# Kernel optimization log

Measured on AMD Instinct MI355X. Metric: run time of the kernel, lower is better.

Reference implementation:

```python
import jax, jax.numpy as jnp
import numpy as np

D_MODEL = 1024
N_HEADS = 16
MIXTURE_FACTOR = 4
LATENT = D_MODEL // MIXTURE_FACTOR  # 256
D_K = D_MODEL // N_HEADS            # 64
B, L = 2, 2048


def setup_inputs() -> dict:
    key = jax.random.key(0)
    ks = jax.random.split(key, 13)
    s_in = 1.0 / np.sqrt(D_MODEL)
    s_lat = 1.0 / np.sqrt(LATENT)
    return {
        "queries": jax.random.normal(ks[0], (B, L, 1, D_MODEL), jnp.float32),
        "keys": jax.random.normal(ks[1], (B, L, 1, D_MODEL), jnp.float32),
        "values": jax.random.normal(ks[2], (B, L, 1, D_MODEL), jnp.float32),
        "Wq": jax.random.normal(ks[3], (D_MODEL, D_MODEL), jnp.float32) * s_in,
        "bq": jnp.zeros((D_MODEL,), jnp.float32),
        "Wd": jax.random.normal(ks[4], (D_MODEL, LATENT), jnp.float32) * s_in,
        "bd": jnp.zeros((LATENT,), jnp.float32),
        "Wk": jax.random.normal(ks[5], (LATENT, D_MODEL), jnp.float32) * s_lat,
        "bk": jnp.zeros((D_MODEL,), jnp.float32),
        "Wv": jax.random.normal(ks[6], (LATENT, D_MODEL), jnp.float32) * s_lat,
        "bv": jnp.zeros((D_MODEL,), jnp.float32),
        "Wo": jax.random.normal(ks[7], (D_MODEL, D_MODEL), jnp.float32) * s_in,
        "bo": jnp.zeros((D_MODEL,), jnp.float32),
    }


def reference(queries, keys, values, Wq, bq, Wd, bd, Wk, bk, Wv, bv, Wo, bo):
    b, l, h_in, e = queries.shape  # h_in == 1, e == d_model
    s = keys.shape[1]
    scale = D_K ** -0.5

    q_flat = queries.reshape(b, l, e)
    Q = (q_flat @ Wq + bq).reshape(b, l, N_HEADS, D_K)

    kv_input = keys.reshape(b, s, e)
    latent = kv_input @ Wd + bd                      # [b, s, latent]
    K = (latent @ Wk + bk).reshape(b, s, N_HEADS, D_K)
    V = (latent @ Wv + bv).reshape(b, s, N_HEADS, D_K)

    scores = jnp.einsum('blhe,bshe->bhls', Q, K) * scale  # [b, h, l, s]
    causal = jnp.triu(jnp.ones((l, s), dtype=bool), k=1)
    scores = jnp.where(causal, -jnp.inf, scores)
    A = jax.nn.softmax(scores, axis=-1)

    out = jnp.einsum('bhls,bshd->blhd', A, V).reshape(b, l, N_HEADS * D_K)
    return out @ Wo + bo
```

## Files before the change

### kernel.cpp

```cpp
#include <hip/hip_runtime.h>
#include <stdint.h>


#define DM 1024
#define NH 16
#define DK 64
#define LL 2048

typedef float  f32x4  __attribute__((ext_vector_type(4)));
typedef __bf16 bf16x8 __attribute__((ext_vector_type(8)));
typedef short  s16x8  __attribute__((ext_vector_type(8)));

__device__ __forceinline__ unsigned short f2bf(float f) {
    union { float f; unsigned int u; } v; v.f = f;
    return (unsigned short)((v.u + 0x7fffu + ((v.u >> 16) & 1u)) >> 16);
}
__device__ __forceinline__ unsigned int pack2(float a, float b) {
    return (unsigned int)f2bf(a) | ((unsigned int)f2bf(b) << 16);
}
__device__ __forceinline__ bf16x8 ld8(const unsigned short* p) {
    s16x8 s = *(const s16x8*)p;
    return __builtin_bit_cast(bf16x8, s);
}
__device__ __forceinline__ void gl16(const void* g, void* l) {
    __builtin_amdgcn_global_load_lds((__attribute__((address_space(1))) void*)(g),
                                     (__attribute__((address_space(3))) void*)(l),
                                     16, 0, 0);
}

__global__ __launch_bounds__(256)
void prep_k(const float* __restrict__ Wq, const float* __restrict__ Wd,
            const float* __restrict__ Wk, const float* __restrict__ Wv,
            const float* __restrict__ Wo, const float* __restrict__ queries,
            const float* __restrict__ keys,
            unsigned short* __restrict__ WqT, unsigned short* __restrict__ WdT,
            unsigned short* __restrict__ WkvT, unsigned short* __restrict__ WoT,
            unsigned short* __restrict__ Qb, unsigned short* __restrict__ Kb) {
    int bid = blockIdx.x;
    const int t = threadIdx.x;

    const float* W; unsigned short* WT; int TK, TN;
    if (bid < 1024)      { W = Wq; WT = WqT;  TK = 1024; TN = 1024; }
    else if (bid < 1280) { bid -= 1024; W = Wd; WT = WdT; TK = 1024; TN = 256; }
    else if (bid < 1536) { bid -= 1280; W = Wk; WT = WkvT; TK = 256; TN = 1024; }
    else if (bid < 1792) { bid -= 1536; W = Wv; WT = WkvT + (size_t)1024 * 256; TK = 256; TN = 1024; }
    else if (bid < 2816) { bid -= 1792; W = Wo; WT = WoT;  TK = 1024; TN = 1024; }
    else {
        bid -= 2816;
        const float* src; unsigned short* dst;
        if (bid < 1024) { src = queries; dst = Qb; }
        else            { bid -= 1024; src = keys; dst = Kb; }
        const size_t base = (size_t)bid * 4096;
#pragma unroll
        for (int i = 0; i < 4; ++i) {
            float4 f = *(const float4*)(src + base + (size_t)(i * 256 + t) * 4);
            uint2 u = { pack2(f.x, f.y), pack2(f.z, f.w) };
            *(uint2*)(dst + base + (size_t)(i * 256 + t) * 4) = u;
        }
        return;
    }
    __shared__ float tile[32][33];
    const int tx = t & 31, ty = t >> 5;
    const int bx = bid % (TK / 32), by = bid / (TK / 32);
    const int k0 = bx * 32, n0 = by * 32;
#pragma unroll
    for (int i = 0; i < 4; ++i)
        tile[ty + 8 * i][tx] = W[(size_t)(k0 + ty + 8 * i) * TN + n0 + tx];
    __syncthreads();
#pragma unroll
    for (int i = 0; i < 4; ++i)
        WT[(size_t)(n0 + ty + 8 * i) * TK + k0 + tx] = f2bf(tile[tx][ty + 8 * i]);
}

template<int MODE>
__global__ __launch_bounds__(256)
void gemm_k(const unsigned short* __restrict__ Ap, const unsigned short* __restrict__ Bt,
            const float* __restrict__ bias, void* __restrict__ Cp,
            const unsigned short* __restrict__ Ap2, const unsigned short* __restrict__ Bt2,
            const float* __restrict__ bias2, void* __restrict__ Cp2,
            int K) {
    __shared__ unsigned short Sh[12288];
    unsigned short* As = Sh;
    unsigned short* Bs = Sh + 8192;

    int bid = blockIdx.x;
    const unsigned short* A;
    const unsigned short* B;
    const float* bs;
    bool second = false;
    int m0, n0;
    if (MODE == 0 && bid >= 512) {
        bid -= 512; A = Ap2; B = Bt2; bs = bias2; second = true;
        const int xcd = bid & 7, s = bid >> 3;
        n0 = (s & 3) * 64; m0 = (xcd * 4 + (s >> 2)) * 128;
    } else {
        A = Ap; B = Bt; bs = bias;
        const int xcd = bid & 7, s = bid >> 3;
        if (MODE == 2) { n0 = (s & 31) * 64; m0 = (xcd * 4 + (s >> 5)) * 128; }
        else           { n0 = (s & 15) * 64; m0 = (xcd * 4 + (s >> 4)) * 128; }
    }

    const int t = threadIdx.x, lane = t & 63, wv = t >> 6;
    const int quad = lane >> 4, l15 = lane & 15;

    const int lr8 = lane >> 3;
    const int g8 = (lane & 7) ^ (lr8 & 7);
    const unsigned short* gA = A + (size_t)(m0 + wv * 32 + lr8) * K + g8 * 8;
    const unsigned short* gB = B + (size_t)(n0 + wv * 16 + lr8) * K + g8 * 8;
    unsigned short* lA = As + wv * 2048;
    unsigned short* lB = Bs + wv * 1024;

    int aoff[4][2], boff[2][2];
#pragma unroll
    for (int i = 0; i < 4; ++i) {
        const int ra = (wv >> 1) * 64 + i * 16 + l15;
#pragma unroll
        for (int ks = 0; ks < 2; ++ks)
            aoff[i][ks] = ra * 64 + (((ks * 4 + quad) ^ (ra & 7)) << 3);
    }
#pragma unroll
    for (int j = 0; j < 2; ++j) {
        const int rb = (wv & 1) * 32 + j * 16 + l15;
#pragma unroll
        for (int ks = 0; ks < 2; ++ks)
            boff[j][ks] = rb * 64 + (((ks * 4 + quad) ^ (rb & 7)) << 3);
    }

    f32x4 acc[4][2] = {};
    for (int kk = 0; kk < K; kk += 64) {
        __syncthreads();
#pragma unroll
        for (int s = 0; s < 4; ++s) gl16(gA + kk + (size_t)s * 8 * K, lA + s * 512);
#pragma unroll
        for (int s = 0; s < 2; ++s) gl16(gB + kk + (size_t)s * 8 * K, lB + s * 512);
        __syncthreads();
#pragma unroll
        for (int ks = 0; ks < 2; ++ks) {
            bf16x8 a[4], b[2];
#pragma unroll
            for (int i = 0; i < 4; ++i) a[i] = ld8(As + aoff[i][ks]);
#pragma unroll
            for (int j = 0; j < 2; ++j) b[j] = ld8(Bs + boff[j][ks]);
#pragma unroll
            for (int i = 0; i < 4; ++i)
#pragma unroll
                for (int j = 0; j < 2; ++j)
                    acc[i][j] = __builtin_amdgcn_mfma_f32_16x16x32_bf16(a[i], b[j], acc[i][j], 0, 0, 0);
        }
    }

    const bool isV = (MODE == 2) && (n0 >= 1024);
    if (!isV) {
#pragma unroll
        for (int j = 0; j < 2; ++j) {
            const int col = n0 + (wv & 1) * 32 + j * 16 + l15;
            const float bvv = bs[col];
            const int cstride = second ? 256 : 1024;
#pragma unroll
            for (int i = 0; i < 2; ++i) {}
#pragma unroll
            for (int i = 0; i < 4; ++i) {
                const int rowb = m0 + (wv >> 1) * 64 + i * 16 + quad * 4;
#pragma unroll
                for (int r = 0; r < 4; ++r) {
                    const float v = acc[i][j][r] + bvv;
                    const int row = rowb + r;
                    if (MODE == 1)
                        ((float*)Cp)[(size_t)row * 1024 + col] = v;
                    else if (second)
                        ((unsigned short*)Cp2)[(size_t)row * 256 + col] = f2bf(v);
                    else
                        ((unsigned short*)Cp)[(size_t)row * 1024 + col] = f2bf(v);
                }
            }
        }
    } else {
        __syncthreads();
        unsigned short* Ld = Sh;
#pragma unroll
        for (int j = 0; j < 2; ++j) {
            const int dloc = (wv & 1) * 32 + j * 16 + l15;
            const float bvv = bias2[(n0 - 1024) + dloc];
#pragma unroll
            for (int i = 0; i < 4; ++i) {
                const int tokb = (wv >> 1) * 64 + i * 16 + quad * 4;
#pragma unroll
                for (int r = 0; r < 4; ++r)
                    Ld[dloc * 136 + tokb + r] = f2bf(acc[i][j][r] + bvv);
            }
        }
        __syncthreads();
        const int dloc = t >> 2;
        const int tk0 = (t & 3) * 32;
        const int bb = m0 >> 11;
        unsigned short* dst = (unsigned short*)Cp2 +
            ((size_t)bb * 1024 + (n0 - 1024) + dloc) * LL + (m0 & (LL - 1)) + tk0;
        const unsigned short* srcp = Ld + dloc * 136 + tk0;
#pragma unroll
        for (int c = 0; c < 4; ++c)
            *(uint4*)(dst + c * 8) = *(const uint4*)(srcp + c * 8);
    }
}

__global__ __launch_bounds__(512)
void attn6_k(const unsigned short* __restrict__ Qp,
             const unsigned short* __restrict__ Kp,
             const unsigned short* __restrict__ VpT,
             unsigned short* __restrict__ Op) {
    __shared__ unsigned short Ks[2][4096];
    __shared__ unsigned short Vs[2][4096];
    __shared__ unsigned short Ps[8][16][72];

    const int t = threadIdx.x, lane = t & 63, wv = t >> 6;
    const int grp = wv >> 2, w4 = wv & 3;
    const int quad = lane >> 4, l15 = lane & 15;

    const int bid = blockIdx.x;
    const int xcd = bid & 7, s = bid >> 3;
    const int pair = s & 15;
    const int combo = xcd * 4 + (s >> 4);
    const int h = combo & 15, b = combo >> 4;

    const int srow = w4 * 16 + (lane >> 3);
    const int g8 = (lane & 7) ^ ((lane >> 3) & 7);
    unsigned short* lK = &Ks[grp][w4 * 1024];
    unsigned short* lV = &Vs[grp][w4 * 1024];
    const int sw = l15 & 7;
    float* cb = (float*)&Ks[0][0];

    for (int tsel = 0; tsel < 2; ++tsel) {
        const int tile = tsel ? (31 - pair) : pair;
        const int q0 = tile * 64;

        const unsigned short* qp = Qp + (size_t)(b * LL + q0 + w4 * 16 + l15) * DM + h * DK;
        const bf16x8 aq0 = ld8(qp + quad * 8);
        const bf16x8 aq1 = ld8(qp + 32 + quad * 8);

        f32x4 acc[4] = {};
        float lrow[4] = {0.f, 0.f, 0.f, 0.f};
        const int rowq = q0 + w4 * 16 + quad * 4;

        const int nit = tile / 2 + 1;
        for (int it = 0; it < nit; ++it) {
            const int c = 2 * it + grp;
            const bool active = (c <= tile);
            const int kt = c * 64;
            __syncthreads();
            if (active) {
                const unsigned short* kg = Kp + (size_t)(b * LL + kt + srow) * DM + h * DK + g8 * 8;
                const unsigned short* vg = VpT + ((size_t)(b * NH + h) * DK + srow) * LL + kt + g8 * 8;
                gl16(kg, lK);             gl16(kg + (size_t)8 * DM, lK + 512);
                gl16(vg, lV);             gl16(vg + (size_t)8 * LL, lV + 512);
            }
            __syncthreads();
            if (!active) continue;

            f32x4 s4[4];
#pragma unroll
            for (int sub = 0; sub < 4; ++sub) {
                const int base = (sub * 16 + l15) * 64;
                f32x4 ss = {};
                bf16x8 b0 = ld8(&Ks[grp][base + ((quad ^ sw) << 3)]);
                ss = __builtin_amdgcn_mfma_f32_16x16x32_bf16(aq0, b0, ss, 0, 0, 0);
                bf16x8 b1 = ld8(&Ks[grp][base + (((4 + quad) ^ sw) << 3)]);
                ss = __builtin_amdgcn_mfma_f32_16x16x32_bf16(aq1, b1, ss, 0, 0, 0);
                s4[sub] = ss;
            }

            if (c == tile) {
#pragma unroll
                for (int sub = 0; sub < 4; ++sub) {
                    const int col = kt + sub * 16 + l15;
#pragma unroll
                    for (int r = 0; r < 4; ++r) {
                        float e = exp2f(fmaf(s4[sub][r], 0.18033688011112042f, -16.0f));
                        if (col > rowq + r) e = 0.f;
                        lrow[r] += e;
                        Ps[wv][quad * 4 + r][sub * 16 + l15] =
                            (unsigned short)(__builtin_bit_cast(unsigned int, e) >> 16);
                    }
                }
            } else {
#pragma unroll
                for (int sub = 0; sub < 4; ++sub) {
#pragma unroll
                    for (int r = 0; r < 4; ++r) {
                        float e = exp2f(fmaf(s4[sub][r], 0.18033688011112042f, -16.0f));
                        lrow[r] += e;
                        Ps[wv][quad * 4 + r][sub * 16 + l15] =
                            (unsigned short)(__builtin_bit_cast(unsigned int, e) >> 16);
                    }
                }
            }

#pragma unroll
            for (int ks = 0; ks < 2; ++ks) {
                bf16x8 ap = ld8(&Ps[wv][l15][ks * 32 + quad * 8]);
#pragma unroll
                for (int sub = 0; sub < 4; ++sub) {
                    bf16x8 bv = ld8(&Vs[grp][(sub * 16 + l15) * 64 + (((ks * 4 + quad) ^ sw) << 3)]);
                    acc[sub] = __builtin_amdgcn_mfma_f32_16x16x32_bf16(ap, bv, acc[sub], 0, 0, 0);
                }
            }
        }

        __syncthreads();
        const int base = (w4 * 64 + lane) * 20;
        if (grp == 1) {
#pragma unroll
            for (int sub = 0; sub < 4; ++sub)
#pragma unroll
                for (int r = 0; r < 4; ++r) cb[base + sub * 4 + r] = acc[sub][r];
#pragma unroll
            for (int r = 0; r < 4; ++r) cb[base + 16 + r] = lrow[r];
        }
        __syncthreads();
        if (grp == 0) {
#pragma unroll
            for (int sub = 0; sub < 4; ++sub)
#pragma unroll
                for (int r = 0; r < 4; ++r) acc[sub][r] += cb[base + sub * 4 + r];
#pragma unroll
            for (int r = 0; r < 4; ++r) {
                lrow[r] += cb[base + 16 + r];
#pragma unroll
                for (int off = 1; off < 16; off <<= 1)
                    lrow[r] += __shfl_xor(lrow[r], off, 64);
                lrow[r] = __builtin_amdgcn_rcpf(lrow[r]);
            }
#pragma unroll
            for (int sub = 0; sub < 4; ++sub)
#pragma unroll
                for (int r = 0; r < 4; ++r)
                    Op[(size_t)(b * LL + rowq + r) * DM + h * DK + sub * 16 + l15] =
                        f2bf(acc[sub][r] * lrow[r]);
        }
    }
}

extern "C" void kernel_launch(void* const* d_in, const int* in_sizes, int n_in,
                              void* d_out, int out_size, void* d_ws, size_t ws_size,
                              hipStream_t stream) {
    const float* queries = (const float*)d_in[0];
    const float* keys    = (const float*)d_in[1];
    const float* Wq = (const float*)d_in[3];  const float* bq = (const float*)d_in[4];
    const float* Wd = (const float*)d_in[5];  const float* bd = (const float*)d_in[6];
    const float* Wk = (const float*)d_in[7];  const float* bk = (const float*)d_in[8];
    const float* Wv = (const float*)d_in[9];  const float* bv = (const float*)d_in[10];
    const float* Wo = (const float*)d_in[11]; const float* bo = (const float*)d_in[12];

    char* ws = (char*)d_ws;
    const size_t MB = 1048576;
    unsigned short* Qp   = (unsigned short*)(ws);
    unsigned short* Kb   = (unsigned short*)(ws + 8 * MB);
    unsigned short* Kp   = (unsigned short*)(ws + 8 * MB);
    unsigned short* Qb   = (unsigned short*)(ws + 16 * MB);
    unsigned short* VpT  = (unsigned short*)(ws + 16 * MB);
    unsigned short* WqT  = (unsigned short*)(ws + 24 * MB);
    unsigned short* Lat  = (unsigned short*)(ws + 26 * MB);
    unsigned short* WdT  = (unsigned short*)(ws + 28 * MB);
    unsigned short* WkvT = (unsigned short*)(ws + 28 * MB + 524288);
    unsigned short* Attn = (unsigned short*)(ws + 24 * MB);
    unsigned short* WoT  = (unsigned short*)(ws + 32 * MB);

    prep_k<<<4864, 256, 0, stream>>>(Wq, Wd, Wk, Wv, Wo, queries, keys,
                                     WqT, WdT, WkvT, WoT, Qb, Kb);
    gemm_k<0><<<640, 256, 0, stream>>>(Qb, WqT, bq, Qp, Kb, WdT, bd, Lat, 1024);
    gemm_k<2><<<1024, 256, 0, stream>>>(Lat, WkvT, bk, Kp, nullptr, nullptr, bv, VpT, 256);
    attn6_k<<<512, 512, 0, stream>>>(Qp, Kp, VpT, Attn);
    gemm_k<1><<<512, 256, 0, stream>>>(Attn, WoT, bo, d_out, nullptr, nullptr, nullptr, nullptr, 1024);
}
```

Before: 205.5 us.

## Double-buffer LDS tiles in GEMM kernel to overlap global loads with MFMA

Replaces the single shared-memory tile in the GEMM kernel with two ping-pong buffers. The load of the next K-slice is issued before the MFMA work on the current one, and the loop keeps one barrier per step instead of two. This is meant to hide global-to-LDS latency behind compute. In exchange, LDS use per block doubles, which may lower occupancy, and the unused cstride code is dropped.

Measured after the change: 198.8 us. 1.03x faster.

```diff
diff --git a/kernel.cpp b/kernel.cpp
--- a/kernel.cpp
+++ b/kernel.cpp
@@ -72,6 +72,33 @@
         WT[(size_t)(n0 + ty + 8 * i) * TK + k0 + tx] = f2bf(tile[tx][ty + 8 * i]);
 }
 
+__device__ __forceinline__ void stage6(const unsigned short* gA, const unsigned short* gB,
+                                       int kk, int K,
+                                       unsigned short* lA, unsigned short* lB) {
+#pragma unroll
+    for (int s = 0; s < 4; ++s) gl16(gA + kk + (size_t)s * 8 * K, lA + s * 512);
+#pragma unroll
+    for (int s = 0; s < 2; ++s) gl16(gB + kk + (size_t)s * 8 * K, lB + s * 512);
+}
+
+__device__ __forceinline__ void mfma16(const unsigned short* As, const unsigned short* Bs,
+                                       const int aoff[4][2], const int boff[2][2],
+                                       f32x4 acc[4][2]) {
+#pragma unroll
+    for (int ks = 0; ks < 2; ++ks) {
+        bf16x8 a[4], b[2];
+#pragma unroll
+        for (int i = 0; i < 4; ++i) a[i] = ld8(As + aoff[i][ks]);
+#pragma unroll
+        for (int j = 0; j < 2; ++j) b[j] = ld8(Bs + boff[j][ks]);
+#pragma unroll
+        for (int i = 0; i < 4; ++i)
+#pragma unroll
+            for (int j = 0; j < 2; ++j)
+                acc[i][j] = __builtin_amdgcn_mfma_f32_16x16x32_bf16(a[i], b[j], acc[i][j], 0, 0, 0);
+    }
+}
+
 template<int MODE>
 __global__ __launch_bounds__(256)
 void gemm_k(const unsigned short* __restrict__ Ap, const unsigned short* __restrict__ Bt,
@@ -79,9 +106,8 @@
             const unsigned short* __restrict__ Ap2, const unsigned short* __restrict__ Bt2,
             const float* __restrict__ bias2, void* __restrict__ Cp2,
             int K) {
-    __shared__ unsigned short Sh[12288];
-    unsigned short* As = Sh;
-    unsigned short* Bs = Sh + 8192;
+    __shared__ unsigned short Sh0[12288];
+    __shared__ unsigned short Sh1[12288];
 
     int bid = blockIdx.x;
     const unsigned short* A;
@@ -107,8 +133,10 @@
     const int g8 = (lane & 7) ^ (lr8 & 7);
     const unsigned short* gA = A + (size_t)(m0 + wv * 32 + lr8) * K + g8 * 8;
     const unsigned short* gB = B + (size_t)(n0 + wv * 16 + lr8) * K + g8 * 8;
-    unsigned short* lA = As + wv * 2048;
-    unsigned short* lB = Bs + wv * 1024;
+    unsigned short* lA0 = Sh0 + wv * 2048;
+    unsigned short* lB0 = Sh0 + 8192 + wv * 1024;
+    unsigned short* lA1 = Sh1 + wv * 2048;
+    unsigned short* lB1 = Sh1 + 8192 + wv * 1024;
 
     int aoff[4][2], boff[2][2];
 #pragma unroll
@@ -127,25 +155,19 @@
     }
 
     f32x4 acc[4][2] = {};
-    for (int kk = 0; kk < K; kk += 64) {
+    const int niter = K >> 6;
+
+    stage6(gA, gB, 0, K, lA0, lB0);
+    __syncthreads();
+    for (int it = 0; it < niter; it += 2) {
+        const int kk = it << 6;
+        if (it + 1 < niter) stage6(gA, gB, kk + 64, K, lA1, lB1);
+        mfma16(Sh0, Sh0 + 8192, aoff, boff, acc);
         __syncthreads();
-#pragma unroll
-        for (int s = 0; s < 4; ++s) gl16(gA + kk + (size_t)s * 8 * K, lA + s * 512);
-#pragma unroll
-        for (int s = 0; s < 2; ++s) gl16(gB + kk + (size_t)s * 8 * K, lB + s * 512);
-        __syncthreads();
-#pragma unroll
-        for (int ks = 0; ks < 2; ++ks) {
-            bf16x8 a[4], b[2];
-#pragma unroll
-            for (int i = 0; i < 4; ++i) a[i] = ld8(As + aoff[i][ks]);
-#pragma unroll
-            for (int j = 0; j < 2; ++j) b[j] = ld8(Bs + boff[j][ks]);
-#pragma unroll
-            for (int i = 0; i < 4; ++i)
-#pragma unroll
-                for (int j = 0; j < 2; ++j)
-                    acc[i][j] = __builtin_amdgcn_mfma_f32_16x16x32_bf16(a[i], b[j], acc[i][j], 0, 0, 0);
+        if (it + 1 < niter) {
+            if (it + 2 < niter) stage6(gA, gB, kk + 128, K, lA0, lB0);
+            mfma16(Sh1, Sh1 + 8192, aoff, boff, acc);
+            __syncthreads();
         }
     }
 
@@ -155,9 +177,6 @@
         for (int j = 0; j < 2; ++j) {
             const int col = n0 + (wv & 1) * 32 + j * 16 + l15;
             const float bvv = bs[col];
-            const int cstride = second ? 256 : 1024;
-#pragma unroll
-            for (int i = 0; i < 2; ++i) {}
 #pragma unroll
             for (int i = 0; i < 4; ++i) {
                 const int rowb = m0 + (wv >> 1) * 64 + i * 16 + quad * 4;
@@ -175,8 +194,7 @@
             }
         }
     } else {
-        __syncthreads();
-        unsigned short* Ld = Sh;
+        unsigned short* Ld = Sh0;
 #pragma unroll
         for (int j = 0; j < 2; ++j) {
             const int dloc = (wv & 1) * 32 + j * 16 + l15;
```

## Use single-wave 64x64 GEMM tiles and compute softmax row sums via MFMA

Applied to the files above, without the earlier changes.

The GEMM kernel moves from 256-thread blocks with 128x64 tiles and a 64-wide K step to one-wave blocks with 64x64 tiles and a 32-wide K step. Grids are doubled and the LDS swizzle and the V-transpose epilogue are adjusted to match. The intent is more blocks and cheaper barriers, at the cost of less data reuse per block and more global loads. Separately, the attention kernel drops its per-element row-sum adds and shuffle reductions and instead gets the softmax denominator from an extra MFMA against a vector of ones.

Result: slower. 216.0 us (+5.1%).

```diff
diff --git a/kernel.cpp b/kernel.cpp
--- a/kernel.cpp
+++ b/kernel.cpp
@@ -73,15 +73,13 @@
 }
 
 template<int MODE>
-__global__ __launch_bounds__(256)
-void gemm_k(const unsigned short* __restrict__ Ap, const unsigned short* __restrict__ Bt,
-            const float* __restrict__ bias, void* __restrict__ Cp,
-            const unsigned short* __restrict__ Ap2, const unsigned short* __restrict__ Bt2,
-            const float* __restrict__ bias2, void* __restrict__ Cp2,
-            int K) {
-    __shared__ unsigned short Sh[12288];
-    unsigned short* As = Sh;
-    unsigned short* Bs = Sh + 8192;
+__global__ __launch_bounds__(64)
+void gemm1w_k(const unsigned short* __restrict__ Ap, const unsigned short* __restrict__ Bt,
+              const float* __restrict__ bias, void* __restrict__ Cp,
+              const unsigned short* __restrict__ Ap2, const unsigned short* __restrict__ Bt2,
+              const float* __restrict__ bias2, void* __restrict__ Cp2,
+              int K) {
+    __shared__ unsigned short Sh[4224];
 
     int bid = blockIdx.x;
     const unsigned short* A;
@@ -89,78 +87,63 @@
     const float* bs;
     bool second = false;
     int m0, n0;
-    if (MODE == 0 && bid >= 512) {
-        bid -= 512; A = Ap2; B = Bt2; bs = bias2; second = true;
+    if (MODE == 0 && bid >= 1024) {
+        bid -= 1024; A = Ap2; B = Bt2; bs = bias2; second = true;
         const int xcd = bid & 7, s = bid >> 3;
-        n0 = (s & 3) * 64; m0 = (xcd * 4 + (s >> 2)) * 128;
+        n0 = (s & 3) * 64; m0 = (xcd * 8 + (s >> 2)) * 64;
     } else {
         A = Ap; B = Bt; bs = bias;
         const int xcd = bid & 7, s = bid >> 3;
-        if (MODE == 2) { n0 = (s & 31) * 64; m0 = (xcd * 4 + (s >> 5)) * 128; }
-        else           { n0 = (s & 15) * 64; m0 = (xcd * 4 + (s >> 4)) * 128; }
-    }
-
-    const int t = threadIdx.x, lane = t & 63, wv = t >> 6;
+        if (MODE == 2) { n0 = (s & 31) * 64; m0 = (xcd * 8 + (s >> 5)) * 64; }
+        else           { n0 = (s & 15) * 64; m0 = (xcd * 8 + (s >> 4)) * 64; }
+    }
+
+    const int lane = threadIdx.x;
     const int quad = lane >> 4, l15 = lane & 15;
 
-    const int lr8 = lane >> 3;
-    const int g8 = (lane & 7) ^ (lr8 & 7);
-    const unsigned short* gA = A + (size_t)(m0 + wv * 32 + lr8) * K + g8 * 8;
-    const unsigned short* gB = B + (size_t)(n0 + wv * 16 + lr8) * K + g8 * 8;
-    unsigned short* lA = As + wv * 2048;
-    unsigned short* lB = Bs + wv * 1024;
-
-    int aoff[4][2], boff[2][2];
+    const int r0 = lane >> 2;
+    const int g = (lane & 3) ^ (r0 & 3) ^ ((r0 >> 2) & 3);
+    const unsigned short* gA = A + (size_t)(m0 + r0) * K + g * 8;
+    const unsigned short* gB = B + (size_t)(n0 + r0) * K + g * 8;
+
+    int aoff[4], boff[4];
 #pragma unroll
     for (int i = 0; i < 4; ++i) {
-        const int ra = (wv >> 1) * 64 + i * 16 + l15;
-#pragma unroll
-        for (int ks = 0; ks < 2; ++ks)
-            aoff[i][ks] = ra * 64 + (((ks * 4 + quad) ^ (ra & 7)) << 3);
-    }
-#pragma unroll
-    for (int j = 0; j < 2; ++j) {
-        const int rb = (wv & 1) * 32 + j * 16 + l15;
-#pragma unroll
-        for (int ks = 0; ks < 2; ++ks)
-            boff[j][ks] = rb * 64 + (((ks * 4 + quad) ^ (rb & 7)) << 3);
-    }
-
-    f32x4 acc[4][2] = {};
-    for (int kk = 0; kk < K; kk += 64) {
-        __syncthreads();
-#pragma unroll
-        for (int s = 0; s < 4; ++s) gl16(gA + kk + (size_t)s * 8 * K, lA + s * 512);
-#pragma unroll
-        for (int s = 0; s < 2; ++s) gl16(gB + kk + (size_t)s * 8 * K, lB + s * 512);
-        __syncthreads();
-#pragma unroll
-        for (int ks = 0; ks < 2; ++ks) {
-            bf16x8 a[4], b[2];
-#pragma unroll
-            for (int i = 0; i < 4; ++i) a[i] = ld8(As + aoff[i][ks]);
-#pragma unroll
-            for (int j = 0; j < 2; ++j) b[j] = ld8(Bs + boff[j][ks]);
-#pragma unroll
-            for (int i = 0; i < 4; ++i)
-#pragma unroll
-                for (int j = 0; j < 2; ++j)
-                    acc[i][j] = __builtin_amdgcn_mfma_f32_16x16x32_bf16(a[i], b[j], acc[i][j], 0, 0, 0);
-        }
+        const int r = i * 16 + l15;
+        const int sw = (r & 3) ^ ((r >> 2) & 3);
+        aoff[i] = r * 32 + ((quad ^ sw) << 3);
+        boff[i] = 2048 + aoff[i];
+    }
+
+    f32x4 acc[4][4] = {};
+    for (int kk = 0; kk < K; kk += 32) {
+#pragma unroll
+        for (int s = 0; s < 4; ++s) gl16(gA + kk + (size_t)s * 16 * K, Sh + s * 512);
+#pragma unroll
+        for (int s = 0; s < 4; ++s) gl16(gB + kk + (size_t)s * 16 * K, Sh + 2048 + s * 512);
+        __syncthreads();
+        bf16x8 a[4], b[4];
+#pragma unroll
+        for (int i = 0; i < 4; ++i) a[i] = ld8(Sh + aoff[i]);
+#pragma unroll
+        for (int j = 0; j < 4; ++j) b[j] = ld8(Sh + boff[j]);
+        __syncthreads();
+#pragma unroll
+        for (int i = 0; i < 4; ++i)
+#pragma unroll
+            for (int j = 0; j < 4; ++j)
+                acc[i][j] = __builtin_amdgcn_mfma_f32_16x16x32_bf16(a[i], b[j], acc[i][j], 0, 0, 0);
     }
 
     const bool isV = (MODE == 2) && (n0 >= 1024);
     if (!isV) {
 #pragma unroll
-        for (int j = 0; j < 2; ++j) {
-            const int col = n0 + (wv & 1) * 32 + j * 16 + l15;
+        for (int j = 0; j < 4; ++j) {
+            const int col = n0 + j * 16 + l15;
             const float bvv = bs[col];
-            const int cstride = second ? 256 : 1024;
-#pragma unroll
-            for (int i = 0; i < 2; ++i) {}
 #pragma unroll
             for (int i = 0; i < 4; ++i) {
-                const int rowb = m0 + (wv >> 1) * 64 + i * 16 + quad * 4;
+                const int rowb = m0 + i * 16 + quad * 4;
 #pragma unroll
                 for (int r = 0; r < 4; ++r) {
                     const float v = acc[i][j][r] + bvv;
@@ -176,34 +159,31 @@
         }
     } else {
         __syncthreads();
-        unsigned short* Ld = Sh;
-#pragma unroll
-        for (int j = 0; j < 2; ++j) {
-            const int dloc = (wv & 1) * 32 + j * 16 + l15;
+#pragma unroll
+        for (int j = 0; j < 4; ++j) {
+            const int dloc = j * 16 + l15;
             const float bvv = bias2[(n0 - 1024) + dloc];
 #pragma unroll
             for (int i = 0; i < 4; ++i) {
-                const int tokb = (wv >> 1) * 64 + i * 16 + quad * 4;
+                const int tokb = i * 16 + quad * 4;
 #pragma unroll
                 for (int r = 0; r < 4; ++r)
-                    Ld[dloc * 136 + tokb + r] = f2bf(acc[i][j][r] + bvv);
-            }
-        }
-        __syncthreads();
-        const int dloc = t >> 2;
-        const int tk0 = (t & 3) * 32;
+                    Sh[dloc * 66 + tokb + r] = f2bf(acc[i][j][r] + bvv);
+            }
+        }
+        __syncthreads();
         const int bb = m0 >> 11;
         unsigned short* dst = (unsigned short*)Cp2 +
-            ((size_t)bb * 1024 + (n0 - 1024) + dloc) * LL + (m0 & (LL - 1)) + tk0;
-        const unsigned short* srcp = Ld + dloc * 136 + tk0;
-#pragma unroll
-        for (int c = 0; c < 4; ++c)
+            ((size_t)bb * 1024 + (n0 - 1024) + lane) * LL + (m0 & (LL - 1));
+        const unsigned short* srcp = Sh + lane * 66;
+#pragma unroll
+        for (int c = 0; c < 8; ++c)
             *(uint4*)(dst + c * 8) = *(const uint4*)(srcp + c * 8);
     }
 }
 
 __global__ __launch_bounds__(512)
-void attn6_k(const unsigned short* __restrict__ Qp,
+void attn7_k(const unsigned short* __restrict__ Qp,
              const unsigned short* __restrict__ Kp,
              const unsigned short* __restrict__ VpT,
              unsigned short* __restrict__ Op) {
@@ -228,6 +208,10 @@
     const int sw = l15 & 7;
     float* cb = (float*)&Ks[0][0];
 
+    const s16x8 ones_s = {(short)0x3F80, (short)0x3F80, (short)0x3F80, (short)0x3F80,
+                          (short)0x3F80, (short)0x3F80, (short)0x3F80, (short)0x3F80};
+    const bf16x8 ones = __builtin_bit_cast(bf16x8, ones_s);
+
     for (int tsel = 0; tsel < 2; ++tsel) {
         const int tile = tsel ? (31 - pair) : pair;
         const int q0 = tile * 64;
@@ -237,7 +221,7 @@
         const bf16x8 aq1 = ld8(qp + 32 + quad * 8);
 
         f32x4 acc[4] = {};
-        float lrow[4] = {0.f, 0.f, 0.f, 0.f};
+        f32x4 acc5 = {};
         const int rowq = q0 + w4 * 16 + quad * 4;
 
         const int nit = tile / 2 + 1;
@@ -275,7 +259,6 @@
                     for (int r = 0; r < 4; ++r) {
                         float e = exp2f(fmaf(s4[sub][r], 0.18033688011112042f, -16.0f));
                         if (col > rowq + r) e = 0.f;
-                        lrow[r] += e;
                         Ps[wv][quad * 4 + r][sub * 16 + l15] =
                             (unsigned short)(__builtin_bit_cast(unsigned int, e) >> 16);
                     }
@@ -286,7 +269,6 @@
 #pragma unroll
                     for (int r = 0; r < 4; ++r) {
                         float e = exp2f(fmaf(s4[sub][r], 0.18033688011112042f, -16.0f));
-                        lrow[r] += e;
                         Ps[wv][quad * 4 + r][sub * 16 + l15] =
                             (unsigned short)(__builtin_bit_cast(unsigned int, e) >> 16);
                     }
@@ -296,6 +278,7 @@
 #pragma unroll
             for (int ks = 0; ks < 2; ++ks) {
                 bf16x8 ap = ld8(&Ps[wv][l15][ks * 32 + quad * 8]);
+                acc5 = __builtin_amdgcn_mfma_f32_16x16x32_bf16(ap, ones, acc5, 0, 0, 0);
 #pragma unroll
                 for (int sub = 0; sub < 4; ++sub) {
                     bf16x8 bv = ld8(&Vs[grp][(sub * 16 + l15) * 64 + (((ks * 4 + quad) ^ sw) << 3)]);
@@ -312,7 +295,7 @@
 #pragma unroll
                 for (int r = 0; r < 4; ++r) cb[base + sub * 4 + r] = acc[sub][r];
 #pragma unroll
-            for (int r = 0; r < 4; ++r) cb[base + 16 + r] = lrow[r];
+            for (int r = 0; r < 4; ++r) cb[base + 16 + r] = acc5[r];
         }
         __syncthreads();
         if (grp == 0) {
@@ -320,20 +303,16 @@
             for (int sub = 0; sub < 4; ++sub)
 #pragma unroll
                 for (int r = 0; r < 4; ++r) acc[sub][r] += cb[base + sub * 4 + r];
-#pragma unroll
-            for (int r = 0; r < 4; ++r) {
-                lrow[r] += cb[base + 16 + r];
-#pragma unroll
-                for (int off = 1; off < 16; off <<= 1)
-                    lrow[r] += __shfl_xor(lrow[r], off, 64);
-                lrow[r] = __builtin_amdgcn_rcpf(lrow[r]);
-            }
+            float inv[4];
+#pragma unroll
+            for (int r = 0; r < 4; ++r)
+                inv[r] = __builtin_amdgcn_rcpf(acc5[r] + cb[base + 16 + r]);
 #pragma unroll
             for (int sub = 0; sub < 4; ++sub)
 #pragma unroll
                 for (int r = 0; r < 4; ++r)
                     Op[(size_t)(b * LL + rowq + r) * DM + h * DK + sub * 16 + l15] =
-                        f2bf(acc[sub][r] * lrow[r]);
+                        f2bf(acc[sub][r] * inv[r]);
         }
     }
 }
@@ -365,8 +344,8 @@
 
     prep_k<<<4864, 256, 0, stream>>>(Wq, Wd, Wk, Wv, Wo, queries, keys,
                                      WqT, WdT, WkvT, WoT, Qb, Kb);
-    gemm_k<0><<<640, 256, 0, stream>>>(Qb, WqT, bq, Qp, Kb, WdT, bd, Lat, 1024);
-    gemm_k<2><<<1024, 256, 0, stream>>>(Lat, WkvT, bk, Kp, nullptr, nullptr, bv, VpT, 256);
-    attn6_k<<<512, 512, 0, stream>>>(Qp, Kp, VpT, Attn);
-    gemm_k<1><<<512, 256, 0, stream>>>(Attn, WoT, bo, d_out, nullptr, nullptr, nullptr, nullptr, 1024);
-}
+    gemm1w_k<0><<<1280, 64, 0, stream>>>(Qb, WqT, bq, Qp, Kb, WdT, bd, Lat, 1024);
+    gemm1w_k<2><<<2048, 64, 0, stream>>>(Lat, WkvT, bk, Kp, nullptr, nullptr, bv, VpT, 256);
+    attn7_k<<<512, 512, 0, stream>>>(Qp, Kp, VpT, Attn);
+    gemm1w_k<1><<<1024, 64, 0, stream>>>(Attn, WoT, bo, d_out, nullptr, nullptr, nullptr, nullptr, 1024);
+}
```
